# Optimization experiments

Hardware: AMD Instinct MI355X
Metric: run time of the kernel (lower is better)

Reference implementation:

```python
import jax, jax.numpy as jnp
import numpy as np

SCALE = 1.0 / np.sqrt(256.0)  # 1/sqrt(hidden_dim)


def setup_inputs() -> dict:
    key = jax.random.key(0)
    ks = jax.random.split(key, 9)
    N, C, H, W = 32, 256, 32, 32
    D, T = 256, 512
    s = lambda k, shape, fan: jax.random.normal(k, shape, jnp.float32) / np.sqrt(fan)
    return {
        "x": jax.random.normal(ks[0], (N, C, H, W), jnp.float32),
        "t": jax.random.normal(ks[1], (N, T), jnp.float32),
        "W_t": s(ks[2], (C, T), T),
        "b_t": jnp.zeros((C,), jnp.float32),
        "Wq": s(ks[3], (D, C), C),
        "Wk": s(ks[4], (D, C), C),
        "Wv": s(ks[5], (D, C), C),
        "Wp": s(ks[6], (C, D), D),
        "bp": jnp.zeros((C,), jnp.float32),
    }


def reference(x, t, W_t, b_t, Wq, Wk, Wv, Wp, bp):
    N, C, H, W = x.shape
    h = x
    # time embedding: Linear + ReLU, broadcast over spatial dims
    temb = jax.nn.relu(t @ W_t.T + b_t)  # [N, C]
    x = x + temb[:, :, None, None]
    # transpose(1,3): [N, C, H, W] -> [N, W, H, C]
    xc = jnp.transpose(x, (0, 3, 2, 1))
    q = xc @ Wq.T  # [N, W, H, D]
    k = xc @ Wk.T
    v = xc @ Wv.T
    # full spatial attention scores: [N, W, H, w, h]
    qk = jnp.einsum('NWHd,Nwhd->NWHwh', q, k) * SCALE
    qk = jax.nn.softmax(qk.reshape(N, W, H, W * H), axis=-1)
    qk = qk.reshape(N, W, H, W, H)
    out = jnp.einsum('NWHwh,Nwhd->NWHd', qk, v)  # [N, W, H, D]
    out = out @ Wp.T + bp  # [N, W, H, C]
    out = jnp.transpose(out, (0, 3, 2, 1))  # [N, C, H, W]
    return out + h
```

## Files before the change

### kernel.cpp

```cpp
#include <hip/hip_runtime.h>

#define NB 32
#define CD 256
#define SS 1024
#define DD 256
#define TT 512
#define SCALE 0.0625f

typedef __attribute__((ext_vector_type(8))) short s16x8;
typedef __attribute__((ext_vector_type(4))) short s16x4;
typedef __attribute__((ext_vector_type(4))) float f32x4;
typedef __attribute__((ext_vector_type(16))) float f32x16;

__device__ __forceinline__ unsigned short f2bf(float f) {
  unsigned u = __builtin_bit_cast(unsigned, f);
  u = (u + 0x7FFFu + ((u >> 16) & 1u)) >> 16;
  return (unsigned short)u;
}
__device__ __forceinline__ float bf2f(unsigned short h) {
  return __builtin_bit_cast(float, ((unsigned)h) << 16);
}

__global__ __launch_bounds__(256) void k_misc(const float* __restrict__ t,
    const float* __restrict__ Wt, const float* __restrict__ bt, float* __restrict__ temb,
    const float* __restrict__ wq, const float* __restrict__ wk,
    const float* __restrict__ wv, const float* __restrict__ wp,
    unsigned short* __restrict__ dst) {
  const int b = blockIdx.x;
  if (b < 1024) {
    const int i = b * 256 + threadIdx.x;
    const int which = i >> 16, off = i & 65535;
    const float* s = which == 0 ? wq : which == 1 ? wk : which == 2 ? wv : wp;
    dst[i] = f2bf(s[off]);
  } else {
    const int n = b - 1024, c = threadIdx.x;
    const float4* tv = (const float4*)(t + (size_t)n * TT);
    const float4* wvv = (const float4*)(Wt + (size_t)c * TT);
    float acc = 0.f;
#pragma unroll 8
    for (int i = 0; i < TT / 4; ++i) {
      float4 a = tv[i], bb = wvv[i];
      acc += a.x * bb.x + a.y * bb.y + a.z * bb.z + a.w * bb.w;
    }
    acc += bt[c];
    temb[n * CD + c] = fmaxf(acc, 0.f);
  }
}

__global__ __launch_bounds__(256) void k_addT(const float* __restrict__ x,
    const float* __restrict__ temb, unsigned short* __restrict__ xb) {
  __shared__ float tile[32][33];
  const int tx = threadIdx.x & 31, ty = threadIdx.x >> 5;
  const int n = blockIdx.z, s0 = blockIdx.y * 32, c0 = blockIdx.x * 32;
#pragma unroll
  for (int i = 0; i < 4; ++i) {
    const int cc = ty + i * 8;
    tile[cc][tx] = x[((size_t)n * CD + c0 + cc) * SS + s0 + tx] + temb[n * CD + c0 + cc];
  }
  __syncthreads();
  unsigned short* op = xb + ((size_t)n * SS + s0) * CD + c0;
#pragma unroll
  for (int i = 0; i < 4; ++i) {
    const int ss = ty + i * 8;
    op[(size_t)ss * CD + tx] = f2bf(tile[tx][ss]);
  }
}

__global__ __launch_bounds__(256) void k_qkv(const unsigned short* __restrict__ A,
    const unsigned short* __restrict__ wb, unsigned short* __restrict__ qb,
    unsigned short* __restrict__ kb, unsigned short* __restrict__ vtb) {
  __shared__ __attribute__((aligned(16))) unsigned short As[128 * 32];
  __shared__ __attribute__((aligned(16))) unsigned short Bs[128 * 32];
  const int which = blockIdx.z >> 5, n = blockIdx.z & 31;
  const int s0 = blockIdx.x * 128;
  const int d0 = blockIdx.y * 128;
  const unsigned short* B = wb + which * 65536;
  const int tid = threadIdx.x;
  const int lane = tid & 63, wid = tid >> 6;
  const int lo = lane & 15, hi = lane >> 4;
  const int wr = wid >> 1, wc = wid & 1;
  const unsigned short* An = A + (size_t)n * SS * CD;
  f32x4 acc[4][4] = {};
  for (int k0 = 0; k0 < CD; k0 += 32) {
#pragma unroll
    for (int i = 0; i < 2; ++i) {
      const int seg = i * 256 + wid * 64 + lane;
      const int row = seg >> 2, c8 = seg & 3;
      const unsigned short* ga = An + (size_t)(s0 + row) * CD + k0 + c8 * 8;
      __builtin_amdgcn_global_load_lds(
          (const __attribute__((address_space(1))) unsigned int*)(const void*)ga,
          (__attribute__((address_space(3))) unsigned int*)(void*)(As + (size_t)(i * 256 + wid * 64) * 8),
          16, 0, 0);
      const unsigned short* gb = B + (size_t)(d0 + row) * CD + k0 + c8 * 8;
      __builtin_amdgcn_global_load_lds(
          (const __attribute__((address_space(1))) unsigned int*)(const void*)gb,
          (__attribute__((address_space(3))) unsigned int*)(void*)(Bs + (size_t)(i * 256 + wid * 64) * 8),
          16, 0, 0);
    }
    __syncthreads();
    s16x8 a[4], b[4];
#pragma unroll
    for (int mi = 0; mi < 4; ++mi)
      a[mi] = *(const s16x8*)&As[(wr * 64 + mi * 16 + lo) * 32 + hi * 8];
#pragma unroll
    for (int ni = 0; ni < 4; ++ni)
      b[ni] = *(const s16x8*)&Bs[(wc * 64 + ni * 16 + lo) * 32 + hi * 8];
#pragma unroll
    for (int mi = 0; mi < 4; ++mi)
#pragma unroll
      for (int ni = 0; ni < 4; ++ni)
        acc[mi][ni] = __builtin_amdgcn_mfma_f32_16x16x32_bf16(a[mi], b[ni], acc[mi][ni], 0, 0, 0);
    __syncthreads();
  }
  if (which < 2) {
    const float osc = which == 0 ? SCALE : 1.0f;
    unsigned short* On = (which == 0 ? qb : kb) + (size_t)n * SS * DD;
#pragma unroll
    for (int mi = 0; mi < 4; ++mi) {
      const int r0 = s0 + wr * 64 + mi * 16 + hi * 4;
#pragma unroll
      for (int ni = 0; ni < 4; ++ni) {
        const int col = d0 + wc * 64 + ni * 16 + lo;
#pragma unroll
        for (int r = 0; r < 4; ++r)
          On[(size_t)(r0 + r) * DD + col] = f2bf(acc[mi][ni][r] * osc);
      }
    }
  } else {
    unsigned short* On = vtb + (size_t)n * DD * SS;
#pragma unroll
    for (int mi = 0; mi < 4; ++mi) {
      const int r0 = s0 + wr * 64 + mi * 16 + hi * 4;
#pragma unroll
      for (int ni = 0; ni < 4; ++ni) {
        const int col = d0 + wc * 64 + ni * 16 + lo;
        s16x4 v;
#pragma unroll
        for (int r = 0; r < 4; ++r) v[r] = (short)f2bf(acc[mi][ni][r]);
        *(s16x4*)&On[(size_t)col * SS + r0] = v;
      }
    }
  }
}

__global__ __launch_bounds__(256, 2) void k_attn(const unsigned short* __restrict__ qb,
    const unsigned short* __restrict__ kb, const unsigned short* __restrict__ vtb,
    unsigned short* __restrict__ ob) {
  __shared__ __attribute__((aligned(16))) unsigned short lds[29696];
  const int bid = blockIdx.x;
  const int qt = bid & 7, dh = (bid >> 3) & 1, n = bid >> 4;
  const int tid = threadIdx.x, lane = tid & 63, w = tid >> 6;
  const int l31 = lane & 31, h = lane >> 5;
  const int dblk = dh * 128;
  const unsigned short* Kn = kb + (size_t)n * SS * DD;
  const unsigned short* Vn = vtb + ((size_t)n * DD + dblk) * SS;
  unsigned short* Pw = lds + 24576 + w * 1280;
  const int qrow = qt * 128 + w * 32 + l31;

  const unsigned short* Qp = qb + ((size_t)n * SS + qrow) * DD + h * 8;
  s16x8 qf[16];
#pragma unroll
  for (int ks = 0; ks < 16; ++ks) qf[ks] = *(const s16x8*)(Qp + ks * 16);

  f32x16 acc[4] = {};
  float mrun = -3.0e38f, lrun = 0.f;

  auto STAGE = [&](int buf, int jt) {
    const int j0 = jt * 32;
    unsigned short* KsB = lds + buf * 8192;
    unsigned short* VsB = lds + 16384 + buf * 4096;
#pragma unroll
    for (int i = 0; i < 4; ++i) {
      const int idx = i * 256 + w * 64 + lane;
      const int row = idx >> 5, c8 = idx & 31;
      const unsigned short* g = Kn + (size_t)(j0 + row) * DD + ((c8 ^ (row & 7)) << 3);
      __builtin_amdgcn_global_load_lds(
          (const __attribute__((address_space(1))) unsigned int*)(const void*)g,
          (__attribute__((address_space(3))) unsigned int*)(void*)(KsB + (size_t)(i * 256 + w * 64) * 8),
          16, 0, 0);
    }
#pragma unroll
    for (int i = 0; i < 2; ++i) {
      const int idx = i * 256 + w * 64 + lane;
      const int row = idx >> 2, c8 = idx & 3;
      const unsigned short* g = Vn + (size_t)row * SS + j0 + ((c8 ^ ((row >> 1) & 3)) << 3);
      __builtin_amdgcn_global_load_lds(
          (const __attribute__((address_space(1))) unsigned int*)(const void*)g,
          (__attribute__((address_space(3))) unsigned int*)(void*)(VsB + (size_t)(i * 256 + w * 64) * 8),
          16, 0, 0);
    }
  };

  STAGE(0, 0);
  __syncthreads();

  int cur = 0;
#pragma unroll 1
  for (int jt = 0; jt < 32; ++jt) {
    if (jt + 1 < 32) STAGE(cur ^ 1, jt + 1);
    const unsigned short* Ks = lds + cur * 8192;
    const unsigned short* Vs = lds + 16384 + cur * 4096;
    f32x16 sc = {};
    __builtin_amdgcn_s_setprio(1);
#pragma unroll
    for (int ks = 0; ks < 16; ++ks) {
      const s16x8 kf = *(const s16x8*)&Ks[l31 * 256 + ((((ks * 2 + h)) ^ (l31 & 7)) << 3)];
      sc = __builtin_amdgcn_mfma_f32_32x32x16_bf16(kf, qf[ks], sc, 0, 0, 0);
    }
    __builtin_amdgcn_s_setprio(0);
    float pm = sc[0];
#pragma unroll
    for (int i = 1; i < 16; ++i) pm = fmaxf(pm, sc[i]);
    pm = fmaxf(pm, __shfl_xor(pm, 32, 64));
    if (__any(pm > mrun + 8.f)) {
      const float mn = fmaxf(mrun, pm);
      const float corr = __expf(mrun - mn);
      mrun = mn; lrun *= corr;
#pragma unroll
      for (int dc = 0; dc < 4; ++dc)
#pragma unroll
        for (int i = 0; i < 16; ++i) acc[dc][i] *= corr;
    }
#pragma unroll
    for (int i = 0; i < 16; ++i) sc[i] = __expf(sc[i] - mrun);
    lrun += (((sc[0] + sc[1]) + (sc[2] + sc[3])) + ((sc[4] + sc[5]) + (sc[6] + sc[7]))) +
            (((sc[8] + sc[9]) + (sc[10] + sc[11])) + ((sc[12] + sc[13]) + (sc[14] + sc[15])));
#pragma unroll
    for (int t = 0; t < 4; ++t) {
      s16x4 pv;
#pragma unroll
      for (int i = 0; i < 4; ++i) pv[i] = (short)f2bf(sc[t * 4 + i]);
      *(s16x4*)&Pw[l31 * 40 + t * 8 + h * 4] = pv;
    }
    const s16x8 pa0 = *(const s16x8*)&Pw[l31 * 40 + h * 8];
    const s16x8 pa1 = *(const s16x8*)&Pw[l31 * 40 + 16 + h * 8];
    __builtin_amdgcn_s_setprio(1);
#pragma unroll
    for (int dc = 0; dc < 4; ++dc) {
      const s16x8 vf0 = *(const s16x8*)&Vs[(dc * 32 + l31) * 32 + ((h ^ ((l31 >> 1) & 3)) << 3)];
      acc[dc] = __builtin_amdgcn_mfma_f32_32x32x16_bf16(vf0, pa0, acc[dc], 0, 0, 0);
    }
#pragma unroll
    for (int dc = 0; dc < 4; ++dc) {
      const s16x8 vf1 = *(const s16x8*)&Vs[(dc * 32 + l31) * 32 + (((2 + h) ^ ((l31 >> 1) & 3)) << 3)];
      acc[dc] = __builtin_amdgcn_mfma_f32_32x32x16_bf16(vf1, pa1, acc[dc], 0, 0, 0);
    }
    __builtin_amdgcn_s_setprio(0);
    __syncthreads();
    cur ^= 1;
  }
  lrun += __shfl_xor(lrun, 32, 64);
  const float inv = 1.0f / lrun;
  unsigned short* Op = ob + ((size_t)n * SS + qrow) * DD + dblk;
#pragma unroll
  for (int dc = 0; dc < 4; ++dc)
#pragma unroll
    for (int rg = 0; rg < 4; ++rg) {
      s16x4 v;
#pragma unroll
      for (int i = 0; i < 4; ++i) v[i] = (short)f2bf(acc[dc][rg * 4 + i] * inv);
      *(s16x4*)(Op + dc * 32 + rg * 8 + h * 4) = v;
    }
}

__global__ __launch_bounds__(256) void k_proj(const unsigned short* __restrict__ ob,
    const unsigned short* __restrict__ wpb, const float* __restrict__ bp,
    const float* __restrict__ x, float* __restrict__ out) {
  __shared__ __attribute__((aligned(16))) unsigned short As[128 * 32];
  __shared__ __attribute__((aligned(16))) unsigned short Bs[128 * 32];
  const int n = blockIdx.z;
  const int s0 = blockIdx.x * 128;
  const int c0 = blockIdx.y * 128;
  const int tid = threadIdx.x;
  const int lane = tid & 63, wid = tid >> 6;
  const int lo = lane & 15, hi = lane >> 4;
  const int wr = wid >> 1, wc = wid & 1;
  const unsigned short* On = ob + (size_t)n * SS * DD;
  f32x4 acc[4][4] = {};
  for (int k0 = 0; k0 < DD; k0 += 32) {
#pragma unroll
    for (int i = 0; i < 2; ++i) {
      const int seg = i * 256 + wid * 64 + lane;
      const int row = seg >> 2, c8 = seg & 3;
      const unsigned short* ga = wpb + (size_t)(c0 + row) * DD + k0 + c8 * 8;
      __builtin_amdgcn_global_load_lds(
          (const __attribute__((address_space(1))) unsigned int*)(const void*)ga,
          (__attribute__((address_space(3))) unsigned int*)(void*)(As + (size_t)(i * 256 + wid * 64) * 8),
          16, 0, 0);
      const unsigned short* gb = On + (size_t)(s0 + row) * DD + k0 + c8 * 8;
      __builtin_amdgcn_global_load_lds(
          (const __attribute__((address_space(1))) unsigned int*)(const void*)gb,
          (__attribute__((address_space(3))) unsigned int*)(void*)(Bs + (size_t)(i * 256 + wid * 64) * 8),
          16, 0, 0);
    }
    __syncthreads();
    s16x8 a[4], b[4];
#pragma unroll
    for (int mi = 0; mi < 4; ++mi)
      a[mi] = *(const s16x8*)&As[(wr * 64 + mi * 16 + lo) * 32 + hi * 8];
#pragma unroll
    for (int ni = 0; ni < 4; ++ni)
      b[ni] = *(const s16x8*)&Bs[(wc * 64 + ni * 16 + lo) * 32 + hi * 8];
#pragma unroll
    for (int mi = 0; mi < 4; ++mi)
#pragma unroll
      for (int ni = 0; ni < 4; ++ni)
        acc[mi][ni] = __builtin_amdgcn_mfma_f32_16x16x32_bf16(a[mi], b[ni], acc[mi][ni], 0, 0, 0);
    __syncthreads();
  }
#pragma unroll
  for (int mi = 0; mi < 4; ++mi) {
#pragma unroll
    for (int r = 0; r < 4; ++r) {
      const int c = c0 + wr * 64 + mi * 16 + hi * 4 + r;
      const float bpc = bp[c];
      const size_t base = ((size_t)n * CD + c) * SS;
#pragma unroll
      for (int ni = 0; ni < 4; ++ni) {
        const int s = s0 + wc * 64 + ni * 16 + lo;
        out[base + s] = acc[mi][ni][r] + bpc + x[base + s];
      }
    }
  }
}

extern "C" void kernel_launch(void* const* d_in, const int* in_sizes, int n_in,
                              void* d_out, int out_size, void* d_ws, size_t ws_size,
                              hipStream_t stream) {
  const float* x  = (const float*)d_in[0];
  const float* t  = (const float*)d_in[1];
  const float* Wt = (const float*)d_in[2];
  const float* bt = (const float*)d_in[3];
  const float* Wq = (const float*)d_in[4];
  const float* Wk = (const float*)d_in[5];
  const float* Wv = (const float*)d_in[6];
  const float* Wp = (const float*)d_in[7];
  const float* bp = (const float*)d_in[8];
  char* ws = (char*)d_ws;
  float* temb        = (float*)ws;
  unsigned short* wb = (unsigned short*)(ws + 32768);
  unsigned short* xb = (unsigned short*)(ws + 557056);
  unsigned short* qb = (unsigned short*)(ws + 17334272);
  unsigned short* kb = (unsigned short*)(ws + 34111488);
  unsigned short* vtb = (unsigned short*)(ws + 50888704);
  unsigned short* ob = (unsigned short*)(ws + 67665920);
  float* out = (float*)d_out;

  k_misc<<<1056, 256, 0, stream>>>(t, Wt, bt, temb, Wq, Wk, Wv, Wp, wb);
  k_addT<<<dim3(8, 32, 32), 256, 0, stream>>>(x, temb, xb);
  k_qkv<<<dim3(8, 2, 96), 256, 0, stream>>>(xb, wb, qb, kb, vtb);
  k_attn<<<512, 256, 0, stream>>>(qb, kb, vtb, ob);
  k_proj<<<dim3(8, 2, 32), 256, 0, stream>>>(ob, wb + 196608, bp, x, out);
}
```

Baseline: 144.3 us.

## Split attention over two KV halves with a combine kernel and exp2 softmax

```diff
diff --git a/kernel.cpp b/kernel.cpp
--- a/kernel.cpp
+++ b/kernel.cpp
@@ -1,11 +1,12 @@
 #include <hip/hip_runtime.h>
+#include <hip/hip_bf16.h>
 
 #define NB 32
 #define CD 256
 #define SS 1024
 #define DD 256
 #define TT 512
-#define SCALE 0.0625f
+#define QSCALE 0.09016844f
 
 typedef __attribute__((ext_vector_type(8))) short s16x8;
 typedef __attribute__((ext_vector_type(4))) short s16x4;
@@ -20,6 +21,17 @@
 __device__ __forceinline__ float bf2f(unsigned short h) {
   return __builtin_bit_cast(float, ((unsigned)h) << 16);
 }
+__device__ __forceinline__ unsigned pk2(float a, float b) {
+  float2 f2; f2.x = a; f2.y = b;
+  __hip_bfloat162 h = __float22bfloat162_rn(f2);
+  unsigned u;
+  __builtin_memcpy(&u, &h, 4);
+  return u;
+}
+#define GLOAD16(gp, lp)                                                        \
+  __builtin_amdgcn_global_load_lds(                                            \
+      (const __attribute__((address_space(1))) unsigned int*)(const void*)(gp),\
+      (__attribute__((address_space(3))) unsigned int*)(void*)(lp), 16, 0, 0)
 
 __global__ __launch_bounds__(256) void k_misc(const float* __restrict__ t,
     const float* __restrict__ Wt, const float* __restrict__ bt, float* __restrict__ temb,
@@ -86,16 +98,8 @@
     for (int i = 0; i < 2; ++i) {
       const int seg = i * 256 + wid * 64 + lane;
       const int row = seg >> 2, c8 = seg & 3;
-      const unsigned short* ga = An + (size_t)(s0 + row) * CD + k0 + c8 * 8;
-      __builtin_amdgcn_global_load_lds(
-          (const __attribute__((address_space(1))) unsigned int*)(const void*)ga,
-          (__attribute__((address_space(3))) unsigned int*)(void*)(As + (size_t)(i * 256 + wid * 64) * 8),
-          16, 0, 0);
-      const unsigned short* gb = B + (size_t)(d0 + row) * CD + k0 + c8 * 8;
-      __builtin_amdgcn_global_load_lds(
-          (const __attribute__((address_space(1))) unsigned int*)(const void*)gb,
-          (__attribute__((address_space(3))) unsigned int*)(void*)(Bs + (size_t)(i * 256 + wid * 64) * 8),
-          16, 0, 0);
+      GLOAD16(An + (size_t)(s0 + row) * CD + k0 + c8 * 8, As + (size_t)(i * 256 + wid * 64) * 8);
+      GLOAD16(B + (size_t)(d0 + row) * CD + k0 + c8 * 8, Bs + (size_t)(i * 256 + wid * 64) * 8);
     }
     __syncthreads();
     s16x8 a[4], b[4];
@@ -113,7 +117,7 @@
     __syncthreads();
   }
   if (which < 2) {
-    const float osc = which == 0 ? SCALE : 1.0f;
+    const float osc = which == 0 ? QSCALE : 1.0f;
     unsigned short* On = (which == 0 ? qb : kb) + (size_t)n * SS * DD;
 #pragma unroll
     for (int mi = 0; mi < 4; ++mi) {
@@ -143,18 +147,19 @@
   }
 }
 
-__global__ __launch_bounds__(256, 2) void k_attn(const unsigned short* __restrict__ qb,
+__global__ __launch_bounds__(256, 3) void k_attn(const unsigned short* __restrict__ qb,
     const unsigned short* __restrict__ kb, const unsigned short* __restrict__ vtb,
-    unsigned short* __restrict__ ob) {
-  __shared__ __attribute__((aligned(16))) unsigned short lds[29696];
+    unsigned short* __restrict__ op1, unsigned short* __restrict__ op2,
+    float2* __restrict__ ml) {
+  __shared__ __attribute__((aligned(16))) unsigned short lds[21504];
   const int bid = blockIdx.x;
-  const int qt = bid & 7, dh = (bid >> 3) & 1, n = bid >> 4;
+  const int qt = bid & 7, dh = (bid >> 3) & 1, kv = (bid >> 4) & 1, n = bid >> 5;
   const int tid = threadIdx.x, lane = tid & 63, w = tid >> 6;
   const int l31 = lane & 31, h = lane >> 5;
   const int dblk = dh * 128;
   const unsigned short* Kn = kb + (size_t)n * SS * DD;
   const unsigned short* Vn = vtb + ((size_t)n * DD + dblk) * SS;
-  unsigned short* Pw = lds + 24576 + w * 1280;
+  unsigned short* Pw = lds + 16384 + w * 1280;
   const int qrow = qt * 128 + w * 32 + l31;
 
   const unsigned short* Qp = qb + ((size_t)n * SS + qrow) * DD + h * 8;
@@ -165,56 +170,56 @@
   f32x16 acc[4] = {};
   float mrun = -3.0e38f, lrun = 0.f;
 
-  auto STAGE = [&](int buf, int jt) {
+  auto STAGE_K = [&](int jt) {
     const int j0 = jt * 32;
-    unsigned short* KsB = lds + buf * 8192;
-    unsigned short* VsB = lds + 16384 + buf * 4096;
 #pragma unroll
     for (int i = 0; i < 4; ++i) {
       const int idx = i * 256 + w * 64 + lane;
       const int row = idx >> 5, c8 = idx & 31;
-      const unsigned short* g = Kn + (size_t)(j0 + row) * DD + ((c8 ^ (row & 7)) << 3);
-      __builtin_amdgcn_global_load_lds(
-          (const __attribute__((address_space(1))) unsigned int*)(const void*)g,
-          (__attribute__((address_space(3))) unsigned int*)(void*)(KsB + (size_t)(i * 256 + w * 64) * 8),
-          16, 0, 0);
-    }
+      GLOAD16(Kn + (size_t)(j0 + row) * DD + ((c8 ^ (row & 7)) << 3),
+              lds + (size_t)(i * 256 + w * 64) * 8);
+    }
+  };
+  auto STAGE_V = [&](int buf, int jt) {
+    const int j0 = jt * 32;
+    unsigned short* VsB = lds + 8192 + buf * 4096;
 #pragma unroll
     for (int i = 0; i < 2; ++i) {
       const int idx = i * 256 + w * 64 + lane;
       const int row = idx >> 2, c8 = idx & 3;
-      const unsigned short* g = Vn + (size_t)row * SS + j0 + ((c8 ^ ((row >> 1) & 3)) << 3);
-      __builtin_amdgcn_global_load_lds(
-          (const __attribute__((address_space(1))) unsigned int*)(const void*)g,
-          (__attribute__((address_space(3))) unsigned int*)(void*)(VsB + (size_t)(i * 256 + w * 64) * 8),
-          16, 0, 0);
+      GLOAD16(Vn + (size_t)row * SS + j0 + ((c8 ^ ((row >> 1) & 3)) << 3),
+              VsB + (size_t)(i * 256 + w * 64) * 8);
     }
   };
 
-  STAGE(0, 0);
+  const int t0 = kv * 16, t1 = t0 + 16;
+  STAGE_K(t0);
+  STAGE_V(0, t0);
   __syncthreads();
 
   int cur = 0;
 #pragma unroll 1
-  for (int jt = 0; jt < 32; ++jt) {
-    if (jt + 1 < 32) STAGE(cur ^ 1, jt + 1);
-    const unsigned short* Ks = lds + cur * 8192;
-    const unsigned short* Vs = lds + 16384 + cur * 4096;
+  for (int jt = t0; jt < t1; ++jt) {
     f32x16 sc = {};
     __builtin_amdgcn_s_setprio(1);
 #pragma unroll
     for (int ks = 0; ks < 16; ++ks) {
-      const s16x8 kf = *(const s16x8*)&Ks[l31 * 256 + ((((ks * 2 + h)) ^ (l31 & 7)) << 3)];
+      const s16x8 kf = *(const s16x8*)&lds[l31 * 256 + ((((ks * 2 + h)) ^ (l31 & 7)) << 3)];
       sc = __builtin_amdgcn_mfma_f32_32x32x16_bf16(kf, qf[ks], sc, 0, 0, 0);
     }
     __builtin_amdgcn_s_setprio(0);
+    __syncthreads();
+    if (jt + 1 < t1) {
+      STAGE_K(jt + 1);
+      STAGE_V(cur ^ 1, jt + 1);
+    }
     float pm = sc[0];
 #pragma unroll
     for (int i = 1; i < 16; ++i) pm = fmaxf(pm, sc[i]);
     pm = fmaxf(pm, __shfl_xor(pm, 32, 64));
     if (__any(pm > mrun + 8.f)) {
       const float mn = fmaxf(mrun, pm);
-      const float corr = __expf(mrun - mn);
+      const float corr = exp2f(mrun - mn);
       mrun = mn; lrun *= corr;
 #pragma unroll
       for (int dc = 0; dc < 4; ++dc)
@@ -222,18 +227,19 @@
         for (int i = 0; i < 16; ++i) acc[dc][i] *= corr;
     }
 #pragma unroll
-    for (int i = 0; i < 16; ++i) sc[i] = __expf(sc[i] - mrun);
+    for (int i = 0; i < 16; ++i) sc[i] = exp2f(sc[i] - mrun);
     lrun += (((sc[0] + sc[1]) + (sc[2] + sc[3])) + ((sc[4] + sc[5]) + (sc[6] + sc[7]))) +
             (((sc[8] + sc[9]) + (sc[10] + sc[11])) + ((sc[12] + sc[13]) + (sc[14] + sc[15])));
 #pragma unroll
     for (int t = 0; t < 4; ++t) {
-      s16x4 pv;
-#pragma unroll
-      for (int i = 0; i < 4; ++i) pv[i] = (short)f2bf(sc[t * 4 + i]);
-      *(s16x4*)&Pw[l31 * 40 + t * 8 + h * 4] = pv;
+      uint2 u;
+      u.x = pk2(sc[t * 4 + 0], sc[t * 4 + 1]);
+      u.y = pk2(sc[t * 4 + 2], sc[t * 4 + 3]);
+      *(uint2*)&Pw[l31 * 40 + t * 8 + h * 4] = u;
     }
     const s16x8 pa0 = *(const s16x8*)&Pw[l31 * 40 + h * 8];
     const s16x8 pa1 = *(const s16x8*)&Pw[l31 * 40 + 16 + h * 8];
+    const unsigned short* Vs = lds + 8192 + cur * 4096;
     __builtin_amdgcn_s_setprio(1);
 #pragma unroll
     for (int dc = 0; dc < 4; ++dc) {
@@ -251,16 +257,46 @@
   }
   lrun += __shfl_xor(lrun, 32, 64);
   const float inv = 1.0f / lrun;
-  unsigned short* Op = ob + ((size_t)n * SS + qrow) * DD + dblk;
+  unsigned short* Op = (kv == 0 ? op1 : op2) + ((size_t)n * SS + qrow) * DD + dblk;
 #pragma unroll
   for (int dc = 0; dc < 4; ++dc)
 #pragma unroll
     for (int rg = 0; rg < 4; ++rg) {
-      s16x4 v;
-#pragma unroll
-      for (int i = 0; i < 4; ++i) v[i] = (short)f2bf(acc[dc][rg * 4 + i] * inv);
-      *(s16x4*)(Op + dc * 32 + rg * 8 + h * 4) = v;
-    }
+      uint2 u;
+      u.x = pk2(acc[dc][rg * 4 + 0] * inv, acc[dc][rg * 4 + 1] * inv);
+      u.y = pk2(acc[dc][rg * 4 + 2] * inv, acc[dc][rg * 4 + 3] * inv);
+      *(uint2*)(Op + dc * 32 + rg * 8 + h * 4) = u;
+    }
+  if (h == 0) {
+    float2 v; v.x = mrun; v.y = lrun;
+    ml[(size_t)kv * (NB * SS) + n * SS + qrow] = v;
+  }
+}
+
+__global__ __launch_bounds__(256) void k_comb(const unsigned short* __restrict__ op1,
+    const unsigned short* __restrict__ op2, const float2* __restrict__ ml,
+    unsigned short* __restrict__ ob) {
+  const int b = blockIdx.x;
+  const int n = b >> 7, q = (b & 127) * 8 + (threadIdx.x >> 5);
+  const int d8 = (threadIdx.x & 31) * 8;
+  const float2 a = ml[(size_t)n * SS + q];
+  const float2 c = ml[(size_t)NB * SS + (size_t)n * SS + q];
+  const float M = fmaxf(a.x, c.x);
+  const float w1 = exp2f(a.x - M) * a.y;
+  const float w2 = exp2f(c.x - M) * c.y;
+  const float inv = 1.0f / (w1 + w2);
+  const float a1 = w1 * inv, a2 = w2 * inv;
+  const size_t off = ((size_t)n * SS + q) * DD + d8;
+  const s16x8 o1 = *(const s16x8*)(op1 + off);
+  const s16x8 o2 = *(const s16x8*)(op2 + off);
+  float v[8];
+#pragma unroll
+  for (int i = 0; i < 8; ++i)
+    v[i] = a1 * bf2f((unsigned short)o1[i]) + a2 * bf2f((unsigned short)o2[i]);
+  uint4 u;
+  u.x = pk2(v[0], v[1]); u.y = pk2(v[2], v[3]);
+  u.z = pk2(v[4], v[5]); u.w = pk2(v[6], v[7]);
+  *(uint4*)(ob + off) = u;
 }
 
 __global__ __launch_bounds__(256) void k_proj(const unsigned short* __restrict__ ob,
@@ -282,16 +318,8 @@
     for (int i = 0; i < 2; ++i) {
       const int seg = i * 256 + wid * 64 + lane;
       const int row = seg >> 2, c8 = seg & 3;
-      const unsigned short* ga = wpb + (size_t)(c0 + row) * DD + k0 + c8 * 8;
-      __builtin_amdgcn_global_load_lds(
-          (const __attribute__((address_space(1))) unsigned int*)(const void*)ga,
-          (__attribute__((address_space(3))) unsigned int*)(void*)(As + (size_t)(i * 256 + wid * 64) * 8),
-          16, 0, 0);
-      const unsigned short* gb = On + (size_t)(s0 + row) * DD + k0 + c8 * 8;
-      __builtin_amdgcn_global_load_lds(
-          (const __attribute__((address_space(1))) unsigned int*)(const void*)gb,
-          (__attribute__((address_space(3))) unsigned int*)(void*)(Bs + (size_t)(i * 256 + wid * 64) * 8),
-          16, 0, 0);
+      GLOAD16(wpb + (size_t)(c0 + row) * DD + k0 + c8 * 8, As + (size_t)(i * 256 + wid * 64) * 8);
+      GLOAD16(On + (size_t)(s0 + row) * DD + k0 + c8 * 8, Bs + (size_t)(i * 256 + wid * 64) * 8);
     }
     __syncthreads();
     s16x8 a[4], b[4];
@@ -344,11 +372,15 @@
   unsigned short* kb = (unsigned short*)(ws + 34111488);
   unsigned short* vtb = (unsigned short*)(ws + 50888704);
   unsigned short* ob = (unsigned short*)(ws + 67665920);
+  float2* ml         = (float2*)(ws + 84443136);
+  unsigned short* op1 = xb;
+  unsigned short* op2 = ob;
   float* out = (float*)d_out;
 
   k_misc<<<1056, 256, 0, stream>>>(t, Wt, bt, temb, Wq, Wk, Wv, Wp, wb);
   k_addT<<<dim3(8, 32, 32), 256, 0, stream>>>(x, temb, xb);
   k_qkv<<<dim3(8, 2, 96), 256, 0, stream>>>(xb, wb, qb, kb, vtb);
-  k_attn<<<512, 256, 0, stream>>>(qb, kb, vtb, ob);
+  k_attn<<<1024, 256, 0, stream>>>(qb, kb, vtb, op1, op2, ml);
+  k_comb<<<4096, 256, 0, stream>>>(op1, op2, ml, ob);
   k_proj<<<dim3(8, 2, 32), 256, 0, stream>>>(ob, wb + 196608, bp, x, out);
 }
```

After: 246.6 us. 1.71x slower.
